# Performance work log

Measured on AMD Instinct MI355X. Metric: run time of the kernel, lower is better.

The kernel has to match this reference:

```python
import jax, jax.numpy as jnp
import numpy as np

NUM_HEADS = 8
EPS = 1e-6


def setup_inputs() -> dict:
    key = jax.random.key(0)
    ks = jax.random.split(key, 6)
    B, T, E = 2, 4096, 512
    s = 0.02
    x = jax.random.normal(ks[0], (B, T, E), dtype=jnp.float32)
    Wq = jax.random.normal(ks[1], (E, E), dtype=jnp.float32) * s
    Wk = jax.random.normal(ks[2], (E, E), dtype=jnp.float32) * s
    Wv = jax.random.normal(ks[3], (E, E), dtype=jnp.float32) * s
    Wo = jax.random.normal(ks[4], (E, E), dtype=jnp.float32) * s
    bq = jnp.zeros((E,), jnp.float32)
    bk = jnp.zeros((E,), jnp.float32)
    bv = jnp.zeros((E,), jnp.float32)
    bo = jnp.zeros((E,), jnp.float32)
    return {"x": x, "Wq": Wq, "bq": bq, "Wk": Wk, "bk": bk,
            "Wv": Wv, "bv": bv, "Wo": Wo, "bo": bo}


def _linear(x, W, b):
    # torch nn.Linear: y = x @ W.T + b
    return x @ W.T + b


def _feature_map(x):
    return jax.nn.elu(x) + 1.0


def _linear_attention(x, Wq, bq, Wk, bk, Wv, bv, Wo, bo):
    B, T, E = x.shape
    H = NUM_HEADS
    D = E // H

    def heads(y):  # (B,T,E) -> (T,B,H,D), time-major for scan
        return y.reshape(B, T, H, D).transpose(1, 0, 2, 3)

    q = _feature_map(heads(_linear(x, Wq, bq)))
    k = _feature_map(heads(_linear(x, Wk, bk)))
    v = heads(_linear(x, Wv, bv))

    # Causal linear attention: running KV outer-product state S (B,H,D,D)
    # and running key sum z (B,H,D). Equivalent to the naive
    # cumsum-of-outer-products (B,H,T,D,D) formulation, but O(D^2) state.
    S0 = jnp.zeros((B, H, D, D), x.dtype)
    z0 = jnp.zeros((B, H, D), x.dtype)

    def step(carry, qkv):
        S, z = carry
        qt, kt, vt = qkv  # each (B,H,D)
        S = S + kt[..., :, None] * vt[..., None, :]
        z = z + kt
        num = jnp.einsum('bhd,bhde->bhe', qt, S)
        den = jnp.sum(qt * z, axis=-1) + EPS  # (B,H)
        return (S, z), num / den[..., None]

    _, out = jax.lax.scan(step, (S0, z0), (q, k, v))  # (T,B,H,D)
    out = out.transpose(1, 0, 2, 3).reshape(B, T, E)
    return _linear(out, Wo, bo)


def reference(x, Wq, bq, Wk, bk, Wv, bv, Wo, bo):
    return _linear_attention(x, Wq, bq, Wk, bk, Wv, bv, Wo, bo)
```

## Files before the change

kernel.cpp:

```cpp
#include <hip/hip_runtime.h>
#include <hip/hip_bf16.h>

#define T_SEQ 4096
#define EMB   512
#define NH    8
#define HD    64
#define BATCH 2
#define M_ROWS (BATCH * T_SEQ)
#define NCHUNK 64
#define CS     64
#define BHEADS (BATCH * NH)

using bf16 = __hip_bfloat16;
typedef __attribute__((ext_vector_type(8))) short short8;
typedef __attribute__((ext_vector_type(4))) float floatx4;

__device__ __forceinline__ float bs2f(short s) {
    return __uint_as_float(((unsigned)(unsigned short)s) << 16);
}
__device__ __forceinline__ short f2bs(float f) {
    bf16 h = __float2bfloat16(f);
    return *reinterpret_cast<short*>(&h);
}
__device__ __forceinline__ float load_elem(const bf16* p, size_t i) {
    return __bfloat162float(p[i]);
}
__device__ __forceinline__ void stage8(const bf16* g, short* l) {
    *reinterpret_cast<short8*>(l) = *reinterpret_cast<const short8*>(g);
}
__device__ __forceinline__ void stage8(const float* g, short* l) {
    float4 a = *reinterpret_cast<const float4*>(g);
    float4 b = *reinterpret_cast<const float4*>(g + 4);
    short8 v;
    v[0] = f2bs(a.x); v[1] = f2bs(a.y); v[2] = f2bs(a.z); v[3] = f2bs(a.w);
    v[4] = f2bs(b.x); v[5] = f2bs(b.y); v[6] = f2bs(b.z); v[7] = f2bs(b.w);
    *reinterpret_cast<short8*>(l) = v;
}

__device__ __forceinline__ void gload_lds16(const short* g, short* l) {
    __builtin_amdgcn_global_load_lds(
        (const __attribute__((address_space(1))) void*)g,
        (__attribute__((address_space(3))) void*)l, 16, 0, 0);
}

#define LDSTR 72

__device__ __forceinline__ int probe_mode(const void* x) {
    const uint4* p = (const uint4*)x;
    const int tid = threadIdx.x;
    bool bad = false;
    #pragma unroll
    for (int i = 0; i < 2; ++i) {
        uint4 u = p[tid + i * 256];
        const unsigned w[4] = {u.x, u.y, u.z, u.w};
        #pragma unroll
        for (int k = 0; k < 4; ++k) {
            const float f = __uint_as_float(w[k] << 16);
            if (!(fabsf(f) <= 1e9f)) bad = true;
        }
    }
    return __syncthreads_or(bad ? 1 : 0) ? 1 : 0;
}

template <typename T>
__device__ __forceinline__ void convert_body(
    const void* const* in, short* xb, short* Wb, short* bb, int c)
{
    if (c < 524288) {
        stage8((const T*)in[0] + (size_t)c * 8, xb + (size_t)c * 8);
    } else if (c < 655360) {
        const int c2 = c - 524288;
        const int w = c2 >> 15;
        const int off = (c2 & 32767) * 8;
        const T* src = (const T*)in[w == 0 ? 1 : (w == 1 ? 3 : (w == 2 ? 5 : 7))];
        stage8(src + off, Wb + w * 262144 + off);
    } else if (c < 655616) {
        const int c3 = c - 655360;
        const int bsel = c3 >> 6;
        const int off = (c3 & 63) * 8;
        const T* src = (const T*)in[bsel == 0 ? 2 : (bsel == 1 ? 4 : (bsel == 2 ? 6 : 8))];
        stage8(src + off, bb + bsel * 512 + off);
    }
}

__global__ __launch_bounds__(256) void convert_all(
    const void* x, const void* Wq, const void* bq,
    const void* Wk, const void* bk, const void* Wv, const void* bv,
    const void* Wo, const void* bo,
    short* __restrict__ xb, short* __restrict__ Wb, short* __restrict__ bb)
{
    const void* in[9] = {x, Wq, bq, Wk, bk, Wv, bv, Wo, bo};
    const int mode = probe_mode(x);
    const int c = blockIdx.x * 256 + threadIdx.x;
    if (mode) convert_body<float>(in, xb, Wb, bb, c);
    else      convert_body<bf16>(in, xb, Wb, bb, c);
}

__global__ __launch_bounds__(256) void qkv_gemm_dl(
    const short* __restrict__ xb, const short* __restrict__ Wb,
    const short* __restrict__ bb,
    bf16* __restrict__ Qf, bf16* __restrict__ Kf, bf16* __restrict__ Vf)
{
    const int mtile = blockIdx.x;
    const int ntile = blockIdx.y;
    const int which = ntile >> 2;
    const short* W = Wb + (size_t)which * 262144;
    const bf16* bias = (const bf16*)(bb + which * 512);
    bf16* outp = (which == 0) ? Qf : ((which == 1) ? Kf : Vf);
    const int nbase = (ntile & 3) * 128;
    const int mbase = mtile * 128;

    __shared__ short As[128 * 64];
    __shared__ short Bs[128 * 64];

    const int tid  = threadIdx.x;
    const int wave = tid >> 6, lane = tid & 63;
    const int wm = wave >> 1, wn = wave & 1;
    const int lm = lane & 15, quad = lane >> 4;
    const int srow = lane >> 3;
    const int scol = (lane & 7) * 8;

    floatx4 acc[4][4];
    const floatx4 zero = {0.f, 0.f, 0.f, 0.f};
    #pragma unroll
    for (int mt = 0; mt < 4; ++mt)
        #pragma unroll
        for (int nt = 0; nt < 4; ++nt) acc[mt][nt] = zero;

    for (int kt = 0; kt < EMB; kt += 64) {
        #pragma unroll
        for (int j = 0; j < 4; ++j) {
            const int issue = wave * 4 + j;
            const int row = issue * 8 + srow;
            gload_lds16(xb + (size_t)(mbase + row) * EMB + kt + scol,
                        &As[issue * 512]);
            gload_lds16(W  + (size_t)(nbase + row) * EMB + kt + scol,
                        &Bs[issue * 512]);
        }
        __syncthreads();
        #pragma unroll
        for (int ks = 0; ks < 2; ++ks) {
            short8 af[4], bfr[4];
            #pragma unroll
            for (int mt = 0; mt < 4; ++mt)
                af[mt] = *reinterpret_cast<const short8*>(
                    &As[(wm * 64 + mt * 16 + lm) * 64 + ks * 32 + quad * 8]);
            #pragma unroll
            for (int nt = 0; nt < 4; ++nt)
                bfr[nt] = *reinterpret_cast<const short8*>(
                    &Bs[(wn * 64 + nt * 16 + lm) * 64 + ks * 32 + quad * 8]);
            #pragma unroll
            for (int mt = 0; mt < 4; ++mt)
                #pragma unroll
                for (int nt = 0; nt < 4; ++nt)
                    acc[mt][nt] = __builtin_amdgcn_mfma_f32_16x16x32_bf16(
                        af[mt], bfr[nt], acc[mt][nt], 0, 0, 0);
        }
        __syncthreads();
    }

    #pragma unroll
    for (int nt = 0; nt < 4; ++nt) {
        const int col = nbase + wn * 64 + nt * 16 + lm;
        const float bv_ = load_elem(bias, col & 511);
        const int h = col >> 6, d = col & 63;
        #pragma unroll
        for (int mt = 0; mt < 4; ++mt)
            #pragma unroll
            for (int r = 0; r < 4; ++r) {
                const int row = mbase + wm * 64 + mt * 16 + quad * 4 + r;
                const int b = row >> 12, t = row & (T_SEQ - 1);
                float v = acc[mt][nt][r] + bv_;
                if (which != 2) v = (v > 0.f) ? (v + 1.f) : __expf(v);
                outp[(((size_t)(b * NH + h)) * T_SEQ + t) * HD + d] = __float2bfloat16(v);
            }
    }
}

__global__ __launch_bounds__(256) void chunk_kv(
    const bf16* __restrict__ Kf, const bf16* __restrict__ Vf,
    float* __restrict__ KVt, float* __restrict__ ksum)
{
    const int bh = blockIdx.x >> 6;
    const int c  = blockIdx.x & 63;
    __shared__ short Kt[64 * LDSTR];
    __shared__ short Vt[64 * LDSTR];
    const int tid = threadIdx.x;
    const bf16* kp = Kf + ((size_t)bh * T_SEQ + c * CS) * HD;
    const bf16* vp = Vf + ((size_t)bh * T_SEQ + c * CS) * HD;

    #pragma unroll
    for (int j = 0; j < 2; ++j) {
        const int u = j * 256 + tid;
        const int e0 = u * 8;
        const int s = e0 >> 6, d0 = e0 & 63;
        short8 ku = *reinterpret_cast<const short8*>(kp + e0);
        short8 vu = *reinterpret_cast<const short8*>(vp + e0);
        #pragma unroll
        for (int i = 0; i < 8; ++i) {
            Kt[(d0 + i) * LDSTR + s] = ku[i];
            Vt[(d0 + i) * LDSTR + s] = vu[i];
        }
    }
    __syncthreads();

    const int w = tid >> 6, lane = tid & 63;
    const int lm = lane & 15, quad = lane >> 4;

    floatx4 acc[4];
    const floatx4 zero = {0.f, 0.f, 0.f, 0.f};
    #pragma unroll
    for (int nt = 0; nt < 4; ++nt) acc[nt] = zero;

    #pragma unroll
    for (int ks = 0; ks < 2; ++ks) {
        short8 av = *reinterpret_cast<const short8*>(
            &Vt[(w * 16 + lm) * LDSTR + ks * 32 + quad * 8]);
        #pragma unroll
        for (int nt = 0; nt < 4; ++nt) {
            short8 bk = *reinterpret_cast<const short8*>(
                &Kt[(nt * 16 + lm) * LDSTR + ks * 32 + quad * 8]);
            acc[nt] = __builtin_amdgcn_mfma_f32_16x16x32_bf16(av, bk, acc[nt], 0, 0, 0);
        }
    }

    float* kvout = KVt + ((size_t)bh * NCHUNK + c) * 4096;
    #pragma unroll
    for (int nt = 0; nt < 4; ++nt)
        #pragma unroll
        for (int r = 0; r < 4; ++r) {
            const int dv = w * 16 + quad * 4 + r;
            const int dk = nt * 16 + lm;
            kvout[dv * 64 + dk] = acc[nt][r];
        }

    if (tid < 64) {
        float s = 0.f;
        #pragma unroll 8
        for (int t = 0; t < 64; ++t) s += bs2f(Kt[tid * LDSTR + t]);
        ksum[((size_t)bh * NCHUNK + c) * 64 + tid] = s;
    }
}

__global__ __launch_bounds__(256) void prefix_kv(
    const float* __restrict__ KVt, bf16* __restrict__ KVb,
    float* __restrict__ ksum)
{
    const int bh   = blockIdx.x >> 4;
    const int part = blockIdx.x & 15;
    const int tid  = threadIdx.x;
    const int e    = part * 256 + tid;
    const float* src = KVt + (size_t)bh * NCHUNK * 4096 + e;
    bf16* dst = KVb + (size_t)bh * NCHUNK * 4096 + e;

    float v[64];
    #pragma unroll
    for (int i = 0; i < 64; ++i) v[i] = src[(size_t)i * 4096];
    float s = 0.f;
    #pragma unroll
    for (int i = 0; i < 64; ++i) {
        dst[(size_t)i * 4096] = __float2bfloat16(s);
        s += v[i];
    }

    if (part == 0 && tid < 64) {
        float* zb = ksum + (size_t)bh * NCHUNK * 64 + tid;
        float z = 0.f;
        float zv[64];
        #pragma unroll
        for (int i = 0; i < 64; ++i) zv[i] = zb[(size_t)i * 64];
        #pragma unroll
        for (int i = 0; i < 64; ++i) {
            zb[(size_t)i * 64] = z;
            z += zv[i];
        }
    }
}

__global__ __launch_bounds__(256, 4) void attn_mfma(
    const bf16* __restrict__ Qf, const bf16* __restrict__ Kf,
    const bf16* __restrict__ Vf, const bf16* __restrict__ KVb,
    const float* __restrict__ ksum, bf16* __restrict__ Of)
{
    const int bh = blockIdx.x >> 6;
    const int c  = blockIdx.x & 63;
    const int b  = bh >> 3, h = bh & 7;

    __shared__ short Qs [64 * LDSTR];
    __shared__ short Ksn[64 * LDSTR];
    __shared__ short Vt [64 * LDSTR];
    __shared__ short Ps [64 * LDSTR];
    __shared__ float zprev[64];

    const int tid = threadIdx.x;
    const int w = tid >> 6, lane = tid & 63;
    const int lm = lane & 15, quad = lane >> 4;
    const size_t coff = ((size_t)bh * T_SEQ + c * CS) * HD;
    const bf16* Sb = KVb + ((size_t)bh * NCHUNK + c) * 4096;

    #pragma unroll
    for (int j = 0; j < 2; ++j) {
        const int u  = j * 256 + tid;
        const int e0 = u * 8;
        const int r = e0 >> 6, cc = e0 & 63;
        *reinterpret_cast<short8*>(&Qs [r * LDSTR + cc]) =
            *reinterpret_cast<const short8*>(Qf + coff + e0);
        *reinterpret_cast<short8*>(&Ksn[r * LDSTR + cc]) =
            *reinterpret_cast<const short8*>(Kf + coff + e0);
        short8 vu = *reinterpret_cast<const short8*>(Vf + coff + e0);
        #pragma unroll
        for (int i = 0; i < 8; ++i) Vt[(cc + i) * LDSTR + r] = vu[i];
    }
    if (tid < 64) zprev[tid] = ksum[((size_t)bh * NCHUNK + c) * 64 + tid];
    __syncthreads();

    const floatx4 zero = {0.f, 0.f, 0.f, 0.f};
    short8 aq[2];
    #pragma unroll
    for (int ks = 0; ks < 2; ++ks)
        aq[ks] = *reinterpret_cast<const short8*>(
            &Qs[(w * 16 + lm) * LDSTR + ks * 32 + quad * 8]);

    floatx4 pacc[4];
    #pragma unroll
    for (int nt = 0; nt < 4; ++nt) pacc[nt] = zero;
    #pragma unroll
    for (int ks = 0; ks < 2; ++ks)
        #pragma unroll
        for (int nt = 0; nt < 4; ++nt) {
            short8 bk = *reinterpret_cast<const short8*>(
                &Ksn[(nt * 16 + lm) * LDSTR + ks * 32 + quad * 8]);
            pacc[nt] = __builtin_amdgcn_mfma_f32_16x16x32_bf16(aq[ks], bk, pacc[nt], 0, 0, 0);
        }

    float tot[4] = {0.f, 0.f, 0.f, 0.f};
    #pragma unroll
    for (int nt = 0; nt < 4; ++nt)
        #pragma unroll
        for (int r = 0; r < 4; ++r) {
            const int t = w * 16 + quad * 4 + r;
            const int s = nt * 16 + lm;
            const float m = (s <= t) ? pacc[nt][r] : 0.f;
            Ps[t * LDSTR + s] = f2bs(m);
            tot[r] += m;
        }
    #pragma unroll
    for (int r = 0; r < 4; ++r) {
        const int t = w * 16 + quad * 4 + r;
        #pragma unroll
        for (int j = 0; j < 4; ++j) {
            const int d = lm + j * 16;
            tot[r] += bs2f(Qs[t * LDSTR + d]) * zprev[d];
        }
    }
    #pragma unroll
    for (int mask = 1; mask < 16; mask <<= 1)
        #pragma unroll
        for (int r = 0; r < 4; ++r) tot[r] += __shfl_xor(tot[r], mask);
    float rdenl[4];
    #pragma unroll
    for (int r = 0; r < 4; ++r) rdenl[r] = 1.f / (tot[r] + 1e-6f);

    floatx4 oacc[4];
    #pragma unroll
    for (int nt = 0; nt < 4; ++nt) oacc[nt] = zero;
    #pragma unroll
    for (int ks = 0; ks < 2; ++ks)
        #pragma unroll
        for (int nt = 0; nt < 4; ++nt) {
            short8 bs = *reinterpret_cast<const short8*>(
                Sb + (nt * 16 + lm) * 64 + ks * 32 + quad * 8);
            oacc[nt] = __builtin_amdgcn_mfma_f32_16x16x32_bf16(aq[ks], bs, oacc[nt], 0, 0, 0);
        }

    #pragma unroll
    for (int ks = 0; ks < 2; ++ks) {
        short8 ap = *reinterpret_cast<const short8*>(
            &Ps[(w * 16 + lm) * LDSTR + ks * 32 + quad * 8]);
        #pragma unroll
        for (int nt = 0; nt < 4; ++nt) {
            short8 bv = *reinterpret_cast<const short8*>(
                &Vt[(nt * 16 + lm) * LDSTR + ks * 32 + quad * 8]);
            oacc[nt] = __builtin_amdgcn_mfma_f32_16x16x32_bf16(ap, bv, oacc[nt], 0, 0, 0);
        }
    }

    #pragma unroll
    for (int nt = 0; nt < 4; ++nt)
        #pragma unroll
        for (int r = 0; r < 4; ++r) {
            const int t  = w * 16 + quad * 4 + r;
            const int dv = nt * 16 + lm;
            const int tg = c * CS + t;
            Of[((size_t)(b * T_SEQ + tg)) * EMB + h * HD + dv] =
                __float2bfloat16(oacc[nt][r] * rdenl[r]);
        }
}

__global__ __launch_bounds__(256) void out_proj_dl(
    const void* __restrict__ xprobe,
    const short* __restrict__ A, const short* __restrict__ Wb,
    const short* __restrict__ bb, void* __restrict__ out)
{
    const int mode = probe_mode(xprobe);

    const int mbase = blockIdx.x * 128;
    const int nbase = blockIdx.y * 128;
    const short* W = Wb + (size_t)3 * 262144;
    const bf16* bias = (const bf16*)(bb + 3 * 512);

    __shared__ short As[128 * 64];
    __shared__ short Bs[128 * 64];

    const int tid  = threadIdx.x;
    const int wave = tid >> 6, lane = tid & 63;
    const int wm = wave >> 1, wn = wave & 1;
    const int lm = lane & 15, quad = lane >> 4;
    const int srow = lane >> 3;
    const int scol = (lane & 7) * 8;

    floatx4 acc[4][4];
    const floatx4 zero = {0.f, 0.f, 0.f, 0.f};
    #pragma unroll
    for (int mt = 0; mt < 4; ++mt)
        #pragma unroll
        for (int nt = 0; nt < 4; ++nt) acc[mt][nt] = zero;

    for (int kt = 0; kt < EMB; kt += 64) {
        #pragma unroll
        for (int j = 0; j < 4; ++j) {
            const int issue = wave * 4 + j;
            const int row = issue * 8 + srow;
            gload_lds16(A + (size_t)(mbase + row) * EMB + kt + scol,
                        &As[issue * 512]);
            gload_lds16(W + (size_t)(nbase + row) * EMB + kt + scol,
                        &Bs[issue * 512]);
        }
        __syncthreads();
        #pragma unroll
        for (int ks = 0; ks < 2; ++ks) {
            short8 af[4], bfr[4];
            #pragma unroll
            for (int mt = 0; mt < 4; ++mt)
                af[mt] = *reinterpret_cast<const short8*>(
                    &As[(wm * 64 + mt * 16 + lm) * 64 + ks * 32 + quad * 8]);
            #pragma unroll
            for (int nt = 0; nt < 4; ++nt)
                bfr[nt] = *reinterpret_cast<const short8*>(
                    &Bs[(wn * 64 + nt * 16 + lm) * 64 + ks * 32 + quad * 8]);
            #pragma unroll
            for (int mt = 0; mt < 4; ++mt)
                #pragma unroll
                for (int nt = 0; nt < 4; ++nt)
                    acc[mt][nt] = __builtin_amdgcn_mfma_f32_16x16x32_bf16(
                        af[mt], bfr[nt], acc[mt][nt], 0, 0, 0);
        }
        __syncthreads();
    }

    #pragma unroll
    for (int nt = 0; nt < 4; ++nt) {
        const int col = nbase + wn * 64 + nt * 16 + lm;
        const float bv_ = load_elem(bias, col);
        #pragma unroll
        for (int mt = 0; mt < 4; ++mt)
            #pragma unroll
            for (int r = 0; r < 4; ++r) {
                const int row = mbase + wm * 64 + mt * 16 + quad * 4 + r;
                const float v = acc[mt][nt][r] + bv_;
                if (mode) ((float*)out)[(size_t)row * EMB + col] = v;
                else      ((bf16*)out)[(size_t)row * EMB + col] = __float2bfloat16(v);
            }
    }
}

extern "C" void kernel_launch(void* const* d_in, const int* in_sizes, int n_in,
                              void* d_out, int out_size, void* d_ws, size_t ws_size,
                              hipStream_t stream)
{
    bf16* Qf = (bf16*)((char*)d_ws + 64);
    bf16* Kf = Qf + 4194304;
    bf16* Vf = Kf + 4194304;
    float* KVt = (float*)(Vf + 4194304);
    short* xb = (short*)KVt;
    float* ks = KVt + 4194304;
    bf16* Of = (bf16*)(ks + 65536);
    short* Wb = (short*)(Of + 4194304);
    short* bb = Wb + 1048576;
    bf16* KVb = (bf16*)(bb + 2048);

    convert_all<<<dim3(2561), 256, 0, stream>>>(
        d_in[0], d_in[1], d_in[2], d_in[3], d_in[4],
        d_in[5], d_in[6], d_in[7], d_in[8], xb, Wb, bb);

    qkv_gemm_dl<<<dim3(64, 12), 256, 0, stream>>>(xb, Wb, bb, Qf, Kf, Vf);
    chunk_kv<<<dim3(BHEADS * NCHUNK), 256, 0, stream>>>(Kf, Vf, KVt, ks);
    prefix_kv<<<dim3(BHEADS * 16), 256, 0, stream>>>(KVt, KVb, ks);
    attn_mfma<<<dim3(BHEADS * NCHUNK), 256, 0, stream>>>(Qf, Kf, Vf, KVb, ks, Of);

    out_proj_dl<<<dim3(64, 4), 256, 0, stream>>>(
        d_in[0], (const short*)Of, Wb, bb, d_out);
}
```

Before: 161.1 us.

## Fuse chunk KV, prefix scan and attention into one cooperative kernel

Replaces the three launches (chunk_kv, prefix_kv, attn_mfma) with a single cooperative kernel that uses grid-wide syncs between the phases. K and V tiles stay in shared memory from the chunk-state phase into the attention phase, so they are not reloaded, and two kernel launches disappear. The prefix scan loops are also split into smaller register batches to lower register pressure. The cost is two grid barriers, and all 1024 blocks must be co-resident; if the cooperative launch fails, the code falls back to the old three-kernel path.

```diff
diff --git a/kernel.cpp b/kernel.cpp
--- a/kernel.cpp
+++ b/kernel.cpp
@@ -1,5 +1,8 @@
 #include <hip/hip_runtime.h>
 #include <hip/hip_bf16.h>
+#include <hip/hip_cooperative_groups.h>
+
+namespace cg = cooperative_groups;
 
 #define T_SEQ 4096
 #define EMB   512
@@ -177,6 +180,209 @@
     }
 }
 
+__global__ __launch_bounds__(256, 4) void chunk_attn_fused(
+    const bf16* __restrict__ Qf, const bf16* __restrict__ Kf,
+    const bf16* __restrict__ Vf, float* __restrict__ KVt,
+    float* __restrict__ ksum, bf16* __restrict__ KVb,
+    bf16* __restrict__ Of)
+{
+    __shared__ short lds[4 * 64 * LDSTR + 128];
+    short* Ksn = lds;
+    short* Vt  = lds + 64 * LDSTR;
+    short* Qs  = lds + 2 * 64 * LDSTR;
+    short* Ps  = lds + 3 * 64 * LDSTR;
+    float* zprev = (float*)(lds + 4 * 64 * LDSTR);
+    short* Kt = Qs;
+
+    const int bh = blockIdx.x >> 6;
+    const int c  = blockIdx.x & 63;
+    const int b  = bh >> 3, h = bh & 7;
+    const int tid = threadIdx.x;
+    const int w = tid >> 6, lane = tid & 63;
+    const int lm = lane & 15, quad = lane >> 4;
+    const size_t coff = ((size_t)bh * T_SEQ + c * CS) * HD;
+    const floatx4 zero = {0.f, 0.f, 0.f, 0.f};
+
+    {
+        const bf16* kp = Kf + coff;
+        const bf16* vp = Vf + coff;
+        #pragma unroll
+        for (int j = 0; j < 2; ++j) {
+            const int u = j * 256 + tid;
+            const int e0 = u * 8;
+            const int s = e0 >> 6, d0 = e0 & 63;
+            short8 ku = *reinterpret_cast<const short8*>(kp + e0);
+            short8 vu = *reinterpret_cast<const short8*>(vp + e0);
+            *reinterpret_cast<short8*>(&Ksn[s * LDSTR + d0]) = ku;
+            #pragma unroll
+            for (int i = 0; i < 8; ++i) {
+                Kt[(d0 + i) * LDSTR + s] = ku[i];
+                Vt[(d0 + i) * LDSTR + s] = vu[i];
+            }
+        }
+        __syncthreads();
+
+        floatx4 acc[4];
+        #pragma unroll
+        for (int nt = 0; nt < 4; ++nt) acc[nt] = zero;
+        #pragma unroll
+        for (int ks = 0; ks < 2; ++ks) {
+            short8 av = *reinterpret_cast<const short8*>(
+                &Vt[(w * 16 + lm) * LDSTR + ks * 32 + quad * 8]);
+            #pragma unroll
+            for (int nt = 0; nt < 4; ++nt) {
+                short8 bk = *reinterpret_cast<const short8*>(
+                    &Kt[(nt * 16 + lm) * LDSTR + ks * 32 + quad * 8]);
+                acc[nt] = __builtin_amdgcn_mfma_f32_16x16x32_bf16(av, bk, acc[nt], 0, 0, 0);
+            }
+        }
+        float* kvout = KVt + ((size_t)bh * NCHUNK + c) * 4096;
+        #pragma unroll
+        for (int nt = 0; nt < 4; ++nt)
+            #pragma unroll
+            for (int r = 0; r < 4; ++r)
+                kvout[(w * 16 + quad * 4 + r) * 64 + nt * 16 + lm] = acc[nt][r];
+
+        if (tid < 64) {
+            float s = 0.f;
+            #pragma unroll 8
+            for (int t = 0; t < 64; ++t) s += bs2f(Kt[tid * LDSTR + t]);
+            ksum[((size_t)bh * NCHUNK + c) * 64 + tid] = s;
+        }
+    }
+
+    cg::this_grid().sync();
+
+    if (blockIdx.x < 256) {
+        const int bh2 = blockIdx.x >> 4, part = blockIdx.x & 15;
+        const int e = part * 256 + tid;
+        const float* src = KVt + (size_t)bh2 * NCHUNK * 4096 + e;
+        bf16* dst = KVb + (size_t)bh2 * NCHUNK * 4096 + e;
+        float s = 0.f;
+        #pragma unroll
+        for (int cb = 0; cb < 2; ++cb) {
+            float v[32];
+            #pragma unroll
+            for (int i = 0; i < 32; ++i) v[i] = src[(size_t)(cb * 32 + i) * 4096];
+            #pragma unroll
+            for (int i = 0; i < 32; ++i) {
+                dst[(size_t)(cb * 32 + i) * 4096] = __float2bfloat16(s);
+                s += v[i];
+            }
+        }
+        if (part == 0 && tid < 64) {
+            float* zb = ksum + (size_t)bh2 * NCHUNK * 64 + tid;
+            float z = 0.f;
+            #pragma unroll
+            for (int cb = 0; cb < 4; ++cb) {
+                float zv[16];
+                #pragma unroll
+                for (int i = 0; i < 16; ++i) zv[i] = zb[(size_t)(cb * 16 + i) * 64];
+                #pragma unroll
+                for (int i = 0; i < 16; ++i) {
+                    zb[(size_t)(cb * 16 + i) * 64] = z;
+                    z += zv[i];
+                }
+            }
+        }
+    }
+
+    cg::this_grid().sync();
+
+    const bf16* Sb = KVb + ((size_t)bh * NCHUNK + c) * 4096;
+    #pragma unroll
+    for (int j = 0; j < 2; ++j) {
+        const int u  = j * 256 + tid;
+        const int e0 = u * 8;
+        const int r = e0 >> 6, cc = e0 & 63;
+        *reinterpret_cast<short8*>(&Qs[r * LDSTR + cc]) =
+            *reinterpret_cast<const short8*>(Qf + coff + e0);
+    }
+    if (tid < 64) zprev[tid] = ksum[((size_t)bh * NCHUNK + c) * 64 + tid];
+    __syncthreads();
+
+    short8 aq[2];
+    #pragma unroll
+    for (int ks = 0; ks < 2; ++ks)
+        aq[ks] = *reinterpret_cast<const short8*>(
+            &Qs[(w * 16 + lm) * LDSTR + ks * 32 + quad * 8]);
+
+    floatx4 pacc[4];
+    #pragma unroll
+    for (int nt = 0; nt < 4; ++nt) pacc[nt] = zero;
+    #pragma unroll
+    for (int ks = 0; ks < 2; ++ks)
+        #pragma unroll
+        for (int nt = 0; nt < 4; ++nt) {
+            short8 bk = *reinterpret_cast<const short8*>(
+                &Ksn[(nt * 16 + lm) * LDSTR + ks * 32 + quad * 8]);
+            pacc[nt] = __builtin_amdgcn_mfma_f32_16x16x32_bf16(aq[ks], bk, pacc[nt], 0, 0, 0);
+        }
+
+    float tot[4] = {0.f, 0.f, 0.f, 0.f};
+    #pragma unroll
+    for (int nt = 0; nt < 4; ++nt)
+        #pragma unroll
+        for (int r = 0; r < 4; ++r) {
+            const int t = w * 16 + quad * 4 + r;
+            const int s = nt * 16 + lm;
+            const float m = (s <= t) ? pacc[nt][r] : 0.f;
+            Ps[t * LDSTR + s] = f2bs(m);
+            tot[r] += m;
+        }
+    #pragma unroll
+    for (int r = 0; r < 4; ++r) {
+        const int t = w * 16 + quad * 4 + r;
+        #pragma unroll
+        for (int j = 0; j < 4; ++j) {
+            const int d = lm + j * 16;
+            tot[r] += bs2f(Qs[t * LDSTR + d]) * zprev[d];
+        }
+    }
+    #pragma unroll
+    for (int mask = 1; mask < 16; mask <<= 1)
+        #pragma unroll
+        for (int r = 0; r < 4; ++r) tot[r] += __shfl_xor(tot[r], mask);
+    float rdenl[4];
+    #pragma unroll
+    for (int r = 0; r < 4; ++r) rdenl[r] = 1.f / (tot[r] + 1e-6f);
+
+    floatx4 oacc[4];
+    #pragma unroll
+    for (int nt = 0; nt < 4; ++nt) oacc[nt] = zero;
+    #pragma unroll
+    for (int ks = 0; ks < 2; ++ks)
+        #pragma unroll
+        for (int nt = 0; nt < 4; ++nt) {
+            short8 bs = *reinterpret_cast<const short8*>(
+                Sb + (nt * 16 + lm) * 64 + ks * 32 + quad * 8);
+            oacc[nt] = __builtin_amdgcn_mfma_f32_16x16x32_bf16(aq[ks], bs, oacc[nt], 0, 0, 0);
+        }
+
+    #pragma unroll
+    for (int ks = 0; ks < 2; ++ks) {
+        short8 ap = *reinterpret_cast<const short8*>(
+            &Ps[(w * 16 + lm) * LDSTR + ks * 32 + quad * 8]);
+        #pragma unroll
+        for (int nt = 0; nt < 4; ++nt) {
+            short8 bv = *reinterpret_cast<const short8*>(
+                &Vt[(nt * 16 + lm) * LDSTR + ks * 32 + quad * 8]);
+            oacc[nt] = __builtin_amdgcn_mfma_f32_16x16x32_bf16(ap, bv, oacc[nt], 0, 0, 0);
+        }
+    }
+
+    #pragma unroll
+    for (int nt = 0; nt < 4; ++nt)
+        #pragma unroll
+        for (int r = 0; r < 4; ++r) {
+            const int t  = w * 16 + quad * 4 + r;
+            const int dv = nt * 16 + lm;
+            const int tg = c * CS + t;
+            Of[((size_t)(b * T_SEQ + tg)) * EMB + h * HD + dv] =
+                __float2bfloat16(oacc[nt][r] * rdenl[r]);
+        }
+}
+
 __global__ __launch_bounds__(256) void chunk_kv(
     const bf16* __restrict__ Kf, const bf16* __restrict__ Vf,
     float* __restrict__ KVt, float* __restrict__ ksum)
@@ -228,11 +434,8 @@
     #pragma unroll
     for (int nt = 0; nt < 4; ++nt)
         #pragma unroll
-        for (int r = 0; r < 4; ++r) {
-            const int dv = w * 16 + quad * 4 + r;
-            const int dk = nt * 16 + lm;
-            kvout[dv * 64 + dk] = acc[nt][r];
-        }
+        for (int r = 0; r < 4; ++r)
+            kvout[(w * 16 + quad * 4 + r) * 64 + nt * 16 + lm] = acc[nt][r];
 
     if (tid < 64) {
         float s = 0.f;
@@ -253,26 +456,32 @@
     const float* src = KVt + (size_t)bh * NCHUNK * 4096 + e;
     bf16* dst = KVb + (size_t)bh * NCHUNK * 4096 + e;
 
-    float v[64];
-    #pragma unroll
-    for (int i = 0; i < 64; ++i) v[i] = src[(size_t)i * 4096];
     float s = 0.f;
     #pragma unroll
-    for (int i = 0; i < 64; ++i) {
-        dst[(size_t)i * 4096] = __float2bfloat16(s);
-        s += v[i];
+    for (int cb = 0; cb < 2; ++cb) {
+        float v[32];
+        #pragma unroll
+        for (int i = 0; i < 32; ++i) v[i] = src[(size_t)(cb * 32 + i) * 4096];
+        #pragma unroll
+        for (int i = 0; i < 32; ++i) {
+            dst[(size_t)(cb * 32 + i) * 4096] = __float2bfloat16(s);
+            s += v[i];
+        }
     }
 
     if (part == 0 && tid < 64) {
         float* zb = ksum + (size_t)bh * NCHUNK * 64 + tid;
         float z = 0.f;
-        float zv[64];
-        #pragma unroll
-        for (int i = 0; i < 64; ++i) zv[i] = zb[(size_t)i * 64];
-        #pragma unroll
-        for (int i = 0; i < 64; ++i) {
-            zb[(size_t)i * 64] = z;
-            z += zv[i];
+        #pragma unroll
+        for (int cb = 0; cb < 4; ++cb) {
+            float zv[16];
+            #pragma unroll
+            for (int i = 0; i < 16; ++i) zv[i] = zb[(size_t)(cb * 16 + i) * 64];
+            #pragma unroll
+            for (int i = 0; i < 16; ++i) {
+                zb[(size_t)(cb * 16 + i) * 64] = z;
+                z += zv[i];
+            }
         }
     }
 }
@@ -494,9 +703,21 @@
         d_in[5], d_in[6], d_in[7], d_in[8], xb, Wb, bb);
 
     qkv_gemm_dl<<<dim3(64, 12), 256, 0, stream>>>(xb, Wb, bb, Qf, Kf, Vf);
-    chunk_kv<<<dim3(BHEADS * NCHUNK), 256, 0, stream>>>(Kf, Vf, KVt, ks);
-    prefix_kv<<<dim3(BHEADS * 16), 256, 0, stream>>>(KVt, KVb, ks);
-    attn_mfma<<<dim3(BHEADS * NCHUNK), 256, 0, stream>>>(Qf, Kf, Vf, KVb, ks, Of);
+
+    {
+        const bf16* Qfc = Qf; const bf16* Kfc = Kf; const bf16* Vfc = Vf;
+        float* KVtc = KVt; float* ksc = ks; bf16* KVbc = KVb; bf16* Ofc = Of;
+        void* cargs[7] = {(void*)&Qfc, (void*)&Kfc, (void*)&Vfc,
+                          (void*)&KVtc, (void*)&ksc, (void*)&KVbc, (void*)&Ofc};
+        hipError_t cerr = hipLaunchCooperativeKernel(
+            (const void*)chunk_attn_fused, dim3(BHEADS * NCHUNK), dim3(256),
+            cargs, 0, stream);
+        if (cerr != hipSuccess) {
+            chunk_kv<<<dim3(BHEADS * NCHUNK), 256, 0, stream>>>(Kf, Vf, KVt, ks);
+            prefix_kv<<<dim3(BHEADS * 16), 256, 0, stream>>>(KVt, KVb, ks);
+            attn_mfma<<<dim3(BHEADS * NCHUNK), 256, 0, stream>>>(Qf, Kf, Vf, KVb, ks, Of);
+        }
+    }
 
     out_proj_dl<<<dim3(64, 4), 256, 0, stream>>>(
         d_in[0], (const short*)Of, Wb, bb, d_out);
```

Result: slower. 376.2 us (+133.5%).
